# Optimization experiments

Measured on AMD Instinct MI355X. Metric: run time of the kernel, lower is better.

## Reference

```python
import jax, jax.numpy as jnp
import numpy as np

N_NODES = 50000
N_EDGES = 800000
F_IN = 128
HEADS = 4
C_OUT = 32
NEG_SLOPE = 0.2
BN_EPS = 1e-5


def _add_self_loops(edge_index, edge_attr, n):
    # PyG fill_value='mean': self-loop attr = mean of incoming edge attrs per node (0 if none)
    src, dst = edge_index[0], edge_index[1]
    deg = jax.ops.segment_sum(jnp.ones_like(edge_attr[:, 0]), dst, num_segments=n)
    loop_attr = jax.ops.segment_sum(edge_attr, dst, num_segments=n) / jnp.maximum(deg, 1.0)[:, None]
    loop = jnp.arange(n)
    src2 = jnp.concatenate([src, loop])
    dst2 = jnp.concatenate([dst, loop])
    attr2 = jnp.concatenate([edge_attr, loop_attr], axis=0)
    return src2, dst2, attr2


def _segment_softmax(logits, seg, n):
    m = jax.ops.segment_max(logits, seg, num_segments=n)
    m = jnp.where(jnp.isfinite(m), m, 0.0)
    ex = jnp.exp(logits - m[seg])
    s = jax.ops.segment_sum(ex, seg, num_segments=n)
    return ex / s[seg]


def _gatv2(x, src, dst, eattr, Wl, bl, Wr, br, We, att, bias, n):
    # x: [n, F]; returns [n, HEADS*C_OUT]
    xl = (x @ Wl + bl).reshape(n, HEADS, C_OUT)
    xr = (x @ Wr + br).reshape(n, HEADS, C_OUT)
    ea = (eattr @ We).reshape(-1, HEADS, C_OUT)
    xlj = xl[src]                                   # [E, H, C] gather
    msg = jax.nn.leaky_relu(xlj + xr[dst] + ea, NEG_SLOPE)
    logits = jnp.einsum('ehc,hc->eh', msg, att)     # [E, H]
    alpha = _segment_softmax(logits, dst, n)
    out = jax.ops.segment_sum(xlj * alpha[..., None], dst, num_segments=n)
    return out.reshape(n, HEADS * C_OUT) + bias


def _batchnorm(x, gamma, beta):
    mu = x.mean(axis=0)
    var = x.var(axis=0)
    return gamma * (x - mu) * jax.lax.rsqrt(var + BN_EPS) + beta


def setup_inputs() -> dict:
    key = jax.random.key(0)
    ks = jax.random.split(key, 20)
    HC = HEADS * C_OUT
    s = 0.05
    inp = {
        'emb': jax.random.normal(ks[0], (N_NODES, F_IN), dtype=jnp.float32),
        'edge_index': jax.random.randint(ks[1], (2, N_EDGES), 0, N_NODES, dtype=jnp.int64),
        'edge_weight': jax.random.uniform(ks[2], (N_EDGES, 1), dtype=jnp.float32),
        'Wl1': jax.random.normal(ks[3], (F_IN, HC)) * s,
        'bl1': jnp.zeros((HC,), jnp.float32),
        'Wr1': jax.random.normal(ks[4], (F_IN, HC)) * s,
        'br1': jnp.zeros((HC,), jnp.float32),
        'We1': jax.random.normal(ks[5], (1, HC)) * s,
        'att1': jax.random.normal(ks[6], (HEADS, C_OUT)) * s,
        'bias1': jnp.zeros((HC,), jnp.float32),
        'gamma1': jnp.ones((HC,), jnp.float32),
        'beta1': jnp.zeros((HC,), jnp.float32),
        'Wl2': jax.random.normal(ks[7], (HC, HC)) * s,
        'bl2': jnp.zeros((HC,), jnp.float32),
        'Wr2': jax.random.normal(ks[8], (HC, HC)) * s,
        'br2': jnp.zeros((HC,), jnp.float32),
        'We2': jax.random.normal(ks[9], (1, HC)) * s,
        'att2': jax.random.normal(ks[10], (HEADS, C_OUT)) * s,
        'bias2': jnp.zeros((HC,), jnp.float32),
    }
    return inp


def reference(emb, edge_index, edge_weight, Wl1, bl1, Wr1, br1, We1, att1, bias1,
              gamma1, beta1, Wl2, bl2, Wr2, br2, We2, att2, bias2):
    n = emb.shape[0]
    src, dst, eattr = _add_self_loops(edge_index, edge_weight, n)
    h1 = _gatv2(emb, src, dst, eattr, Wl1, bl1, Wr1, br1, We1, att1, bias1, n)
    h1 = jax.nn.elu(_batchnorm(h1, gamma1, beta1))
    h2 = _gatv2(h1, src, dst, eattr, Wl2, bl2, Wr2, br2, We2, att2, bias2, n)
    # fusion: mean over [input_emb, h1, h2] along stacked axis
    return (emb + h1 + h2) / 3.0
```

## Files before the change

kernel.cpp:

```cpp
#include <hip/hip_runtime.h>
#include <hip/hip_bf16.h>
#include <math.h>

#define N_NODES 50000
#define N_EDGES 800000
#define HC 128
#define SLOT 64
#define CSTRIDE 16

#define BM 128
#define NBX ((N_NODES + BM - 1) / BM)
#define NB_EDGE ((N_EDGES / 4 + 255) / 256)

typedef short bh8 __attribute__((ext_vector_type(8)));
typedef float f4 __attribute__((ext_vector_type(4)));
typedef float f2 __attribute__((ext_vector_type(2)));

__device__ __forceinline__ unsigned int pk2(float a, float b) {
  return (unsigned int)__bfloat16_as_ushort(__float2bfloat16(a)) |
         ((unsigned int)__bfloat16_as_ushort(__float2bfloat16(b)) << 16);
}
__device__ __forceinline__ float blo(unsigned int u) { return __uint_as_float(u << 16); }
__device__ __forceinline__ float bhi(unsigned int u) { return __uint_as_float(u & 0xffff0000u); }

__global__ __launch_bounds__(256) void k_wprep(
    const float* __restrict__ Wl1, const float* __restrict__ Wr1,
    const float* __restrict__ Wl2, const float* __restrict__ Wr2,
    unsigned short* __restrict__ WtAll, int* __restrict__ cursor,
    float* __restrict__ chsum, float* __restrict__ chsq) {
  int gid = blockIdx.x * 256 + threadIdx.x;
  int m = gid >> 14;
  int idx = gid & 16383;
  const float* src = (m == 0) ? Wl1 : (m == 1) ? Wr1 : (m == 2) ? Wl2 : Wr2;
  int k = idx >> 7, n = idx & 127;
  WtAll[((size_t)m * HC + n) * HC + k] =
      __bfloat16_as_ushort(__float2bfloat16(src[k * HC + n]));
  for (int i = gid; i < N_NODES * CSTRIDE; i += 65536) cursor[i] = 0;
  if (gid < HC) { chsum[gid] = 0.f; chsq[gid] = 0.f; }
}

__global__ __launch_bounds__(256) void k_g1prep(
    const float* __restrict__ X, const unsigned short* __restrict__ Wt,
    const float* __restrict__ b0, const float* __restrict__ b1,
    unsigned short* __restrict__ Y0b, float* __restrict__ Y1,
    const int* __restrict__ ei, const float* __restrict__ ew,
    int* __restrict__ cursor, unsigned int* __restrict__ slots) {
  int bid = blockIdx.x;
  int tid = threadIdx.x;
  if (bid >= NBX) {
    int e = ((bid - NBX) * 256 + tid) * 4;
    if (e >= N_EDGES) return;
    int4 s4 = *(const int4*)(ei + e);
    int4 d4 = *(const int4*)(ei + N_EDGES + e);
    float4 w4 = *(const float4*)(ew + e);
    int ss[4] = {s4.x, s4.y, s4.z, s4.w};
    int dd[4] = {d4.x, d4.y, d4.z, d4.w};
    float ww[4] = {w4.x, w4.y, w4.z, w4.w};
    int pos[4];
#pragma unroll
    for (int i = 0; i < 4; ++i) pos[i] = atomicAdd(cursor + dd[i] * CSTRIDE, 1);
#pragma unroll
    for (int i = 0; i < 4; ++i) {
      unsigned int wq = min((unsigned int)(ww[i] * 65536.f + 0.5f), 65535u);
      if (pos[i] < SLOT) {
        slots[(size_t)dd[i] * SLOT + pos[i]] = ((unsigned int)ss[i] << 16) | wq;
      }
    }
    return;
  }
  __shared__ __align__(16) unsigned short Xls[128 * 128];
  int row0 = bid * BM;
  {
    int r = tid >> 1;
    int ks = (tid & 1) * 64;
    int gr = row0 + r;
    const float* xp = X + (size_t)gr * HC + ks;
    int sw = r & 15;
#pragma unroll
    for (int i = 0; i < 4; ++i) {
      float f[16];
      if (gr < N_NODES) {
        *(float4*)&f[0] = *(const float4*)(xp + i * 16);
        *(float4*)&f[4] = *(const float4*)(xp + i * 16 + 4);
        *(float4*)&f[8] = *(const float4*)(xp + i * 16 + 8);
        *(float4*)&f[12] = *(const float4*)(xp + i * 16 + 12);
      } else {
#pragma unroll
        for (int j = 0; j < 16; ++j) f[j] = 0.f;
      }
      int kg = (ks >> 3) + i * 2;
      *(uint4*)&Xls[r * 128 + ((kg ^ sw) * 8)] =
          make_uint4(pk2(f[0], f[1]), pk2(f[2], f[3]), pk2(f[4], f[5]), pk2(f[6], f[7]));
      *(uint4*)&Xls[r * 128 + (((kg + 1) ^ sw) * 8)] =
          make_uint4(pk2(f[8], f[9]), pk2(f[10], f[11]), pk2(f[12], f[13]), pk2(f[14], f[15]));
    }
  }
  __syncthreads();
  int lane = tid & 63;
  int wv = tid >> 6;
  int lrow = lane & 15;
  int lq = lane >> 4;
  int rbase = wv * 32;
  bh8 afr[4][2];
#pragma unroll
  for (int kk = 0; kk < 4; ++kk) {
    int kg = kk * 4 + lq;
    afr[kk][0] = *(const bh8*)&Xls[(rbase + lrow) * 128 + ((kg ^ lrow) * 8)];
    afr[kk][1] = *(const bh8*)&Xls[(rbase + 16 + lrow) * 128 + ((kg ^ lrow) * 8)];
  }
#pragma unroll
  for (int half = 0; half < 2; ++half) {
    const unsigned short* wbase = Wt + half * (HC * HC);
    f4 acc[2][8];
#pragma unroll
    for (int mt = 0; mt < 2; ++mt)
#pragma unroll
      for (int nt = 0; nt < 8; ++nt) acc[mt][nt] = (f4){0.f, 0.f, 0.f, 0.f};
#pragma unroll
    for (int kk = 0; kk < 4; ++kk) {
      int kg = kk * 4 + lq;
#pragma unroll
      for (int nt = 0; nt < 8; ++nt) {
        bh8 b = *(const bh8*)(wbase + (nt * 16 + lrow) * HC + kg * 8);
        acc[0][nt] = __builtin_amdgcn_mfma_f32_16x16x32_bf16(afr[kk][0], b, acc[0][nt], 0, 0, 0);
        acc[1][nt] = __builtin_amdgcn_mfma_f32_16x16x32_bf16(afr[kk][1], b, acc[1][nt], 0, 0, 0);
      }
    }
    const float* bb = half ? b1 : b0;
    float bv[8];
#pragma unroll
    for (int nt = 0; nt < 8; ++nt) bv[nt] = bb[nt * 16 + lrow];
#pragma unroll
    for (int mt = 0; mt < 2; ++mt) {
#pragma unroll
      for (int rr = 0; rr < 4; ++rr) {
        int gr = row0 + rbase + mt * 16 + lq * 4 + rr;
        if (gr < N_NODES) {
          if (half == 0) {
#pragma unroll
            for (int nt = 0; nt < 8; ++nt)
              Y0b[(size_t)gr * HC + nt * 16 + lrow] =
                  __bfloat16_as_ushort(__float2bfloat16(acc[mt][nt][rr] + bv[nt]));
          } else {
#pragma unroll
            for (int nt = 0; nt < 8; ++nt)
              Y1[(size_t)gr * HC + nt * 16 + lrow] = acc[mt][nt][rr] + bv[nt];
          }
        }
      }
    }
  }
}

__global__ __launch_bounds__(256) void k_gemm2(
    const unsigned short* __restrict__ Xb, const unsigned short* __restrict__ Wt,
    const float* __restrict__ b0, const float* __restrict__ b1,
    unsigned char* __restrict__ Y0f8, float* __restrict__ Y1,
    const float* __restrict__ chsum, const float* __restrict__ chsq,
    const float* __restrict__ gamma, const float* __restrict__ beta) {
  __shared__ __align__(16) unsigned short Xls[128 * 128];
  __shared__ __align__(16) unsigned short Wls[128 * 128];
  __shared__ float ssc[HC], ssh[HC];
  int tid = threadIdx.x;
  if (tid < HC) {
    float mu = chsum[tid] * (1.f / N_NODES);
    float var = chsq[tid] * (1.f / N_NODES) - mu * mu;
    float sc = gamma[tid] * rsqrtf(var + 1e-5f);
    ssc[tid] = sc;
    ssh[tid] = beta[tid] - mu * sc;
  }
  __syncthreads();
  int row0 = blockIdx.x * BM;
  {
    int r = tid >> 1;
    int ks = (tid & 1) * 64;
    int gr = row0 + r;
    const unsigned short* xp = Xb + (size_t)gr * HC + ks;
    int sw = r & 15;
#pragma unroll
    for (int i = 0; i < 4; ++i) {
      float f[16];
      if (gr < N_NODES) {
        uint4 ua = *(const uint4*)(xp + i * 16);
        uint4 ub = *(const uint4*)(xp + i * 16 + 8);
        f[0] = blo(ua.x); f[1] = bhi(ua.x); f[2] = blo(ua.y); f[3] = bhi(ua.y);
        f[4] = blo(ua.z); f[5] = bhi(ua.z); f[6] = blo(ua.w); f[7] = bhi(ua.w);
        f[8] = blo(ub.x); f[9] = bhi(ub.x); f[10] = blo(ub.y); f[11] = bhi(ub.y);
        f[12] = blo(ub.z); f[13] = bhi(ub.z); f[14] = blo(ub.w); f[15] = bhi(ub.w);
      } else {
#pragma unroll
        for (int j = 0; j < 16; ++j) f[j] = 0.f;
      }
#pragma unroll
      for (int j = 0; j < 16; ++j) {
        float y = fmaf(f[j], ssc[ks + i * 16 + j], ssh[ks + i * 16 + j]);
        f[j] = (y > 0.f) ? y : (__expf(y) - 1.f);
      }
      int kg = (ks >> 3) + i * 2;
      *(uint4*)&Xls[r * 128 + ((kg ^ sw) * 8)] =
          make_uint4(pk2(f[0], f[1]), pk2(f[2], f[3]), pk2(f[4], f[5]), pk2(f[6], f[7]));
      *(uint4*)&Xls[r * 128 + (((kg + 1) ^ sw) * 8)] =
          make_uint4(pk2(f[8], f[9]), pk2(f[10], f[11]), pk2(f[12], f[13]), pk2(f[14], f[15]));
    }
  }
  int lane = tid & 63;
  int wv = tid >> 6;
  int lrow = lane & 15;
  int lq = lane >> 4;
  int rbase = wv * 32;
#pragma unroll
  for (int half = 0; half < 2; ++half) {
    if (half) __syncthreads();
    {
      int n = tid >> 1;
      int ks = (tid & 1) * 64;
      const unsigned short* wp = Wt + half * (HC * HC) + n * HC + ks;
      int swn = n & 15;
#pragma unroll
      for (int g = 0; g < 8; ++g) {
        uint4 v = *(const uint4*)(wp + g * 8);
        int kg = (ks >> 3) + g;
        *(uint4*)&Wls[n * 128 + ((kg ^ swn) * 8)] = v;
      }
    }
    __syncthreads();
    f4 acc[2][8];
#pragma unroll
    for (int mt = 0; mt < 2; ++mt)
#pragma unroll
      for (int nt = 0; nt < 8; ++nt) acc[mt][nt] = (f4){0.f, 0.f, 0.f, 0.f};
#pragma unroll
    for (int kk = 0; kk < 4; ++kk) {
      int kg = kk * 4 + lq;
      bh8 a0 = *(const bh8*)&Xls[(rbase + lrow) * 128 + ((kg ^ lrow) * 8)];
      bh8 a1 = *(const bh8*)&Xls[(rbase + 16 + lrow) * 128 + ((kg ^ lrow) * 8)];
#pragma unroll
      for (int nt = 0; nt < 8; ++nt) {
        bh8 b = *(const bh8*)&Wls[(nt * 16 + lrow) * 128 + ((kg ^ lrow) * 8)];
        acc[0][nt] = __builtin_amdgcn_mfma_f32_16x16x32_bf16(a0, b, acc[0][nt], 0, 0, 0);
        acc[1][nt] = __builtin_amdgcn_mfma_f32_16x16x32_bf16(a1, b, acc[1][nt], 0, 0, 0);
      }
    }
    const float* bb = half ? b1 : b0;
    float bv[8];
#pragma unroll
    for (int nt = 0; nt < 8; ++nt) bv[nt] = bb[nt * 16 + lrow];
#pragma unroll
    for (int mt = 0; mt < 2; ++mt) {
#pragma unroll
      for (int rr = 0; rr < 4; ++rr) {
        int gr = row0 + rbase + mt * 16 + lq * 4 + rr;
        if (gr < N_NODES) {
          if (half == 0) {
#pragma unroll
            for (int nt = 0; nt < 8; ++nt) {
              float v = acc[mt][nt][rr] + bv[nt];
              int p = __builtin_amdgcn_cvt_pk_fp8_f32(v, v, 0, false);
              Y0f8[(size_t)gr * HC + nt * 16 + lrow] = (unsigned char)(p & 0xff);
            }
          } else {
#pragma unroll
            for (int nt = 0; nt < 8; ++nt)
              Y1[(size_t)gr * HC + nt * 16 + lrow] = acc[mt][nt][rr] + bv[nt];
          }
        }
      }
    }
  }
}

template <int FINAL, int F8>
__global__ __launch_bounds__(256) void k_gat(
    const void* __restrict__ xlv, const float* __restrict__ xr,
    const int* __restrict__ cursor, const unsigned int* __restrict__ slots,
    const float* __restrict__ We, const float* __restrict__ att,
    const float* __restrict__ bias, void* __restrict__ out,
    const float* __restrict__ emb, const unsigned short* __restrict__ h1p,
    const float* __restrict__ chsum, const float* __restrict__ chsq,
    const float* __restrict__ gamma, const float* __restrict__ beta) {
  int g = threadIdx.x >> 5;
  int lane = threadIdx.x & 31;
  int n = blockIdx.x * 8 + g;
  int fi = n * 32 + lane;
  const uint2* xl2 = (const uint2*)xlv;
  const unsigned int* xf = (const unsigned int*)xlv;
  float4 xr4 = ((const float4*)xr)[fi];
  float4 we4 = ((const float4*)We)[lane];
  float4 at4 = ((const float4*)att)[lane];
  int deg = min(cursor[n * CSTRIDE], SLOT);
  int base = n * SLOT;
  int deg32 = min(deg, 32);

  unsigned int ev = (lane < deg32) ? slots[base + lane] : 0u;
  float evw = (float)(ev & 0xffffu) * (1.f / 65536.f);
  float wsum = evw;
#pragma unroll
  for (int m = 16; m >= 1; m >>= 1) wsum += __shfl_xor(wsum, m);

  float l = 0.f;
  float4 o = make_float4(0.f, 0.f, 0.f, 0.f);

  auto decode = [&](uint2 gc) -> float4 {
    float4 xlj;
    if (F8) {
      f2 ab = __builtin_amdgcn_cvt_pk_f32_fp8((int)gc.x, false);
      f2 cd = __builtin_amdgcn_cvt_pk_f32_fp8((int)gc.x, true);
      xlj.x = ab[0]; xlj.y = ab[1]; xlj.z = cd[0]; xlj.w = cd[1];
    } else {
      xlj.x = blo(gc.x); xlj.y = bhi(gc.x);
      xlj.z = blo(gc.y); xlj.w = bhi(gc.y);
    }
    return xlj;
  };
  auto edge_body = [&](float w, uint2 gc, bool valid) {
    float4 xlj = decode(gc);
    float4 v;
    v.x = fmaf(w, we4.x, xlj.x + xr4.x);
    v.y = fmaf(w, we4.y, xlj.y + xr4.y);
    v.z = fmaf(w, we4.z, xlj.z + xr4.z);
    v.w = fmaf(w, we4.w, xlj.w + xr4.w);
    v.x = fmaxf(v.x, 0.2f * v.x);
    v.y = fmaxf(v.y, 0.2f * v.y);
    v.z = fmaxf(v.z, 0.2f * v.z);
    v.w = fmaxf(v.w, 0.2f * v.w);
    float p = v.x * at4.x + v.y * at4.y + v.z * at4.z + v.w * at4.w;
    p += __shfl_xor(p, 1);
    p += __shfl_xor(p, 2);
    p += __shfl_xor(p, 4);
    float e = valid ? __expf(p) : 0.f;
    l += e;
    o.x = fmaf(e, xlj.x, o.x);
    o.y = fmaf(e, xlj.y, o.y);
    o.z = fmaf(e, xlj.z, o.z);
    o.w = fmaf(e, xlj.w, o.w);
  };
  auto fetch = [&](int j, uint2& qq, float& ww) {
    int jc = min(j, deg32 - 1);
    unsigned int evj = __shfl(ev, jc, 32);
    ww = (float)(evj & 0xffffu) * (1.f / 65536.f);
    int s = (int)(evj >> 16);
    if (F8) qq.x = xf[s * 32 + lane];
    else qq = xl2[s * 32 + lane];
  };

  if (deg32 > 0) {
    uint2 q0, q1, q2, q3;
    float w0, w1, w2, w3;
    fetch(0, q0, w0);
    fetch(1, q1, w1);
    fetch(2, q2, w2);
    fetch(3, q3, w3);
    for (int b = 0; b < deg32; b += 4) {
      uint2 c0 = q0, c1 = q1, c2 = q2, c3 = q3;
      float x0 = w0, x1 = w1, x2 = w2, x3 = w3;
      fetch(b + 4, q0, w0);
      fetch(b + 5, q1, w1);
      fetch(b + 6, q2, w2);
      fetch(b + 7, q3, w3);
      edge_body(x0, c0, true);
      edge_body(x1, c1, b + 1 < deg32);
      edge_body(x2, c2, b + 2 < deg32);
      edge_body(x3, c3, b + 3 < deg32);
    }
  }
  if (deg > 32) {
    for (int j = base + 32; j < base + deg; ++j) {
      unsigned int evj = slots[j];
      float w = (float)(evj & 0xffffu) * (1.f / 65536.f);
      wsum += w;
      int s = (int)(evj >> 16);
      uint2 gc;
      if (F8) gc.x = xf[s * 32 + lane];
      else gc = xl2[s * 32 + lane];
      edge_body(w, gc, true);
    }
  }
  {
    float wself = (deg > 0) ? wsum / (float)deg : 0.f;
    uint2 gs;
    if (F8) gs.x = xf[n * 32 + lane];
    else gs = xl2[n * 32 + lane];
    edge_body(wself, gs, true);
  }

  float inv = 1.f / l;
  float4 b4 = ((const float4*)bias)[lane];
  float4 r;
  r.x = fmaf(o.x, inv, b4.x);
  r.y = fmaf(o.y, inv, b4.y);
  r.z = fmaf(o.z, inv, b4.z);
  r.w = fmaf(o.w, inv, b4.w);
  if (FINAL) {
    float4 e4 = ((const float4*)emb)[fi];
    uint2 hh = ((const uint2*)h1p)[fi];
    float4 h4;
    h4.x = blo(hh.x); h4.y = bhi(hh.x); h4.z = blo(hh.y); h4.w = bhi(hh.y);
    float4 cs = ((const float4*)chsum)[lane];
    float4 cq = ((const float4*)chsq)[lane];
    float4 gm = ((const float4*)gamma)[lane];
    float4 bt = ((const float4*)beta)[lane];
    const float invN = 1.f / N_NODES;
    float4 sc4, sh4;
    {
      float mu = cs.x * invN, var = cq.x * invN - mu * mu;
      sc4.x = gm.x * rsqrtf(var + 1e-5f); sh4.x = bt.x - mu * sc4.x;
      mu = cs.y * invN; var = cq.y * invN - mu * mu;
      sc4.y = gm.y * rsqrtf(var + 1e-5f); sh4.y = bt.y - mu * sc4.y;
      mu = cs.z * invN; var = cq.z * invN - mu * mu;
      sc4.z = gm.z * rsqrtf(var + 1e-5f); sh4.z = bt.z - mu * sc4.z;
      mu = cs.w * invN; var = cq.w * invN - mu * mu;
      sc4.w = gm.w * rsqrtf(var + 1e-5f); sh4.w = bt.w - mu * sc4.w;
    }
    float4 h;
    h.x = fmaf(h4.x, sc4.x, sh4.x);
    h.y = fmaf(h4.y, sc4.y, sh4.y);
    h.z = fmaf(h4.z, sc4.z, sh4.z);
    h.w = fmaf(h4.w, sc4.w, sh4.w);
    h.x = (h.x > 0.f) ? h.x : (__expf(h.x) - 1.f);
    h.y = (h.y > 0.f) ? h.y : (__expf(h.y) - 1.f);
    h.z = (h.z > 0.f) ? h.z : (__expf(h.z) - 1.f);
    h.w = (h.w > 0.f) ? h.w : (__expf(h.w) - 1.f);
    const float k3 = 1.f / 3.f;
    r.x = (e4.x + h.x + r.x) * k3;
    r.y = (e4.y + h.y + r.y) * k3;
    r.z = (e4.z + h.z + r.z) * k3;
    r.w = (e4.w + h.w + r.w) * k3;
    ((float4*)out)[fi] = r;
  } else {
    ((uint2*)out)[fi] = make_uint2(pk2(r.x, r.y), pk2(r.z, r.w));
  }
}

#define BN_ROWS 200
__global__ __launch_bounds__(256) void k_bnstats(const unsigned short* __restrict__ h1b,
                                                 float* __restrict__ chsum,
                                                 float* __restrict__ chsq) {
  int c2 = threadIdx.x & 63;
  int g = threadIdx.x >> 6;
  int r0 = blockIdx.x * BN_ROWS;
  float s0 = 0.f, s1 = 0.f, q0 = 0.f, q1 = 0.f;
  const unsigned int* h32 = (const unsigned int*)h1b;
  for (int r = r0 + g; r < r0 + BN_ROWS; r += 4) {
    unsigned int u = h32[(size_t)r * 64 + c2];
    float a = blo(u), b = bhi(u);
    s0 += a; q0 += a * a;
    s1 += b; q1 += b * b;
  }
  __shared__ float sh[256][4];
  sh[threadIdx.x][0] = s0; sh[threadIdx.x][1] = q0;
  sh[threadIdx.x][2] = s1; sh[threadIdx.x][3] = q1;
  __syncthreads();
  if (g == 0) {
    float ts0 = 0.f, tq0 = 0.f, ts1 = 0.f, tq1 = 0.f;
#pragma unroll
    for (int gg = 0; gg < 4; ++gg) {
      ts0 += sh[gg * 64 + c2][0]; tq0 += sh[gg * 64 + c2][1];
      ts1 += sh[gg * 64 + c2][2]; tq1 += sh[gg * 64 + c2][3];
    }
    atomicAdd(chsum + 2 * c2, ts0);
    atomicAdd(chsq + 2 * c2, tq0);
    atomicAdd(chsum + 2 * c2 + 1, ts1);
    atomicAdd(chsq + 2 * c2 + 1, tq1);
  }
}

extern "C" void kernel_launch(void* const* d_in, const int* in_sizes, int n_in,
                              void* d_out, int out_size, void* d_ws, size_t ws_size,
                              hipStream_t stream) {
  const float* emb = (const float*)d_in[0];
  const int* ei = (const int*)d_in[1];
  const float* ew = (const float*)d_in[2];
  const float* Wl1 = (const float*)d_in[3];
  const float* bl1 = (const float*)d_in[4];
  const float* Wr1 = (const float*)d_in[5];
  const float* br1 = (const float*)d_in[6];
  const float* We1 = (const float*)d_in[7];
  const float* att1 = (const float*)d_in[8];
  const float* bias1 = (const float*)d_in[9];
  const float* gamma1 = (const float*)d_in[10];
  const float* beta1 = (const float*)d_in[11];
  const float* Wl2 = (const float*)d_in[12];
  const float* bl2 = (const float*)d_in[13];
  const float* Wr2 = (const float*)d_in[14];
  const float* br2 = (const float*)d_in[15];
  const float* We2 = (const float*)d_in[16];
  const float* att2 = (const float*)d_in[17];
  const float* bias2 = (const float*)d_in[18];
  float* out = (float*)d_out;

  char* wsb = (char*)d_ws;
  size_t off = 0;
  auto alloc = [&](size_t bytes) -> void* {
    void* p = (void*)(wsb + off);
    off += (bytes + 255) & ~(size_t)255;
    return p;
  };
  int* cursor = (int*)alloc((size_t)N_NODES * CSTRIDE * 4);
  float* chsum = (float*)alloc(HC * 4);
  float* chsq = (float*)alloc(HC * 4);
  unsigned short* WtAll = (unsigned short*)alloc((size_t)4 * HC * HC * 2);
  unsigned int* slots = (unsigned int*)alloc((size_t)N_NODES * SLOT * 4);
  unsigned short* xlb = (unsigned short*)alloc((size_t)N_NODES * HC * 2);
  unsigned char* xlf8 = (unsigned char*)alloc((size_t)N_NODES * HC);
  float* xr = (float*)alloc((size_t)N_NODES * HC * 4);
  unsigned short* h1b = (unsigned short*)alloc((size_t)N_NODES * HC * 2);

  k_wprep<<<256, 256, 0, stream>>>(Wl1, Wr1, Wl2, Wr2, WtAll, cursor, chsum, chsq);
  k_g1prep<<<NBX + NB_EDGE, 256, 0, stream>>>(emb, WtAll, bl1, br1, xlb, xr,
                                              ei, ew, cursor, slots);
  k_gat<0, 0><<<N_NODES / 8, 256, 0, stream>>>(xlb, xr, cursor, slots, We1, att1,
                                               bias1, (void*)h1b, nullptr, nullptr,
                                               nullptr, nullptr, nullptr, nullptr);
  k_bnstats<<<N_NODES / BN_ROWS, 256, 0, stream>>>(h1b, chsum, chsq);
  k_gemm2<<<NBX, 256, 0, stream>>>(h1b, WtAll + 2 * HC * HC, bl2, br2, xlf8, xr,
                                   chsum, chsq, gamma1, beta1);
  k_gat<1, 1><<<N_NODES / 8, 256, 0, stream>>>(xlf8, xr, cursor, slots, We2, att2,
                                               bias2, (void*)out, emb, h1b,
                                               chsum, chsq, gamma1, beta1);
}
```

Before: 289.9 us.

## Fuse edge bucketing into GEMM blocks and stage weights in LDS

Removes the separate edge-processing blocks of the first prep kernel. Each GEMM thread now handles 8 edges, issuing its cursor atomics before the X tile load so their latency overlaps with the tile staging, and writing slots afterward. Weight tiles are staged into swizzled shared memory per half instead of being loaded from global memory per MFMA, and A fragments are reloaded from LDS per k-step. LDS usage doubles to 64KB per block, which may limit occupancy, and every GEMM thread now carries the serialized atomic work.

```diff
diff --git a/kernel.cpp b/kernel.cpp
--- a/kernel.cpp
+++ b/kernel.cpp
@@ -10,7 +10,6 @@
 
 #define BM 128
 #define NBX ((N_NODES + BM - 1) / BM)
-#define NB_EDGE ((N_EDGES / 4 + 255) / 256)
 
 typedef short bh8 __attribute__((ext_vector_type(8)));
 typedef float f4 __attribute__((ext_vector_type(4)));
@@ -45,30 +44,28 @@
     unsigned short* __restrict__ Y0b, float* __restrict__ Y1,
     const int* __restrict__ ei, const float* __restrict__ ew,
     int* __restrict__ cursor, unsigned int* __restrict__ slots) {
+  __shared__ __align__(16) unsigned short Xls[128 * 128];
+  __shared__ __align__(16) unsigned short Wls[128 * 128];
   int bid = blockIdx.x;
   int tid = threadIdx.x;
-  if (bid >= NBX) {
-    int e = ((bid - NBX) * 256 + tid) * 4;
-    if (e >= N_EDGES) return;
-    int4 s4 = *(const int4*)(ei + e);
-    int4 d4 = *(const int4*)(ei + N_EDGES + e);
-    float4 w4 = *(const float4*)(ew + e);
-    int ss[4] = {s4.x, s4.y, s4.z, s4.w};
-    int dd[4] = {d4.x, d4.y, d4.z, d4.w};
-    float ww[4] = {w4.x, w4.y, w4.z, w4.w};
-    int pos[4];
-#pragma unroll
-    for (int i = 0; i < 4; ++i) pos[i] = atomicAdd(cursor + dd[i] * CSTRIDE, 1);
-#pragma unroll
-    for (int i = 0; i < 4; ++i) {
-      unsigned int wq = min((unsigned int)(ww[i] * 65536.f + 0.5f), 65535u);
-      if (pos[i] < SLOT) {
-        slots[(size_t)dd[i] * SLOT + pos[i]] = ((unsigned int)ss[i] << 16) | wq;
-      }
-    }
-    return;
-  }
-  __shared__ __align__(16) unsigned short Xls[128 * 128];
+
+  int et = bid * 256 + tid;
+  bool has_e = (et < N_EDGES / 8);
+  int e0 = et * 8;
+  int ss[8], dd[8];
+  float ww[8];
+  int pos[8];
+  if (has_e) {
+    *(int4*)&ss[0] = *(const int4*)(ei + e0);
+    *(int4*)&ss[4] = *(const int4*)(ei + e0 + 4);
+    *(int4*)&dd[0] = *(const int4*)(ei + N_EDGES + e0);
+    *(int4*)&dd[4] = *(const int4*)(ei + N_EDGES + e0 + 4);
+    *(float4*)&ww[0] = *(const float4*)(ew + e0);
+    *(float4*)&ww[4] = *(const float4*)(ew + e0 + 4);
+#pragma unroll
+    for (int i = 0; i < 8; ++i) pos[i] = atomicAdd(cursor + dd[i] * CSTRIDE, 1);
+  }
+
   int row0 = bid * BM;
   {
     int r = tid >> 1;
@@ -95,22 +92,38 @@
           make_uint4(pk2(f[8], f[9]), pk2(f[10], f[11]), pk2(f[12], f[13]), pk2(f[14], f[15]));
     }
   }
-  __syncthreads();
+
+  if (has_e) {
+#pragma unroll
+    for (int i = 0; i < 8; ++i) {
+      unsigned int wq = min((unsigned int)(ww[i] * 65536.f + 0.5f), 65535u);
+      if (pos[i] < SLOT) {
+        slots[(size_t)dd[i] * SLOT + pos[i]] = ((unsigned int)ss[i] << 16) | wq;
+      }
+    }
+  }
+
   int lane = tid & 63;
   int wv = tid >> 6;
   int lrow = lane & 15;
   int lq = lane >> 4;
   int rbase = wv * 32;
-  bh8 afr[4][2];
-#pragma unroll
-  for (int kk = 0; kk < 4; ++kk) {
-    int kg = kk * 4 + lq;
-    afr[kk][0] = *(const bh8*)&Xls[(rbase + lrow) * 128 + ((kg ^ lrow) * 8)];
-    afr[kk][1] = *(const bh8*)&Xls[(rbase + 16 + lrow) * 128 + ((kg ^ lrow) * 8)];
-  }
 #pragma unroll
   for (int half = 0; half < 2; ++half) {
-    const unsigned short* wbase = Wt + half * (HC * HC);
+    if (half) __syncthreads();
+    {
+      int n = tid >> 1;
+      int ks2 = (tid & 1) * 64;
+      const unsigned short* wp = Wt + half * (HC * HC) + n * HC + ks2;
+      int swn = n & 15;
+#pragma unroll
+      for (int g = 0; g < 8; ++g) {
+        uint4 v = *(const uint4*)(wp + g * 8);
+        int kg = (ks2 >> 3) + g;
+        *(uint4*)&Wls[n * 128 + ((kg ^ swn) * 8)] = v;
+      }
+    }
+    __syncthreads();
     f4 acc[2][8];
 #pragma unroll
     for (int mt = 0; mt < 2; ++mt)
@@ -119,11 +132,13 @@
 #pragma unroll
     for (int kk = 0; kk < 4; ++kk) {
       int kg = kk * 4 + lq;
+      bh8 a0 = *(const bh8*)&Xls[(rbase + lrow) * 128 + ((kg ^ lrow) * 8)];
+      bh8 a1 = *(const bh8*)&Xls[(rbase + 16 + lrow) * 128 + ((kg ^ lrow) * 8)];
 #pragma unroll
       for (int nt = 0; nt < 8; ++nt) {
-        bh8 b = *(const bh8*)(wbase + (nt * 16 + lrow) * HC + kg * 8);
-        acc[0][nt] = __builtin_amdgcn_mfma_f32_16x16x32_bf16(afr[kk][0], b, acc[0][nt], 0, 0, 0);
-        acc[1][nt] = __builtin_amdgcn_mfma_f32_16x16x32_bf16(afr[kk][1], b, acc[1][nt], 0, 0, 0);
+        bh8 b = *(const bh8*)&Wls[(nt * 16 + lrow) * 128 + ((kg ^ lrow) * 8)];
+        acc[0][nt] = __builtin_amdgcn_mfma_f32_16x16x32_bf16(a0, b, acc[0][nt], 0, 0, 0);
+        acc[1][nt] = __builtin_amdgcn_mfma_f32_16x16x32_bf16(a1, b, acc[1][nt], 0, 0, 0);
       }
     }
     const float* bb = half ? b1 : b0;
@@ -506,8 +521,8 @@
   unsigned short* h1b = (unsigned short*)alloc((size_t)N_NODES * HC * 2);
 
   k_wprep<<<256, 256, 0, stream>>>(Wl1, Wr1, Wl2, Wr2, WtAll, cursor, chsum, chsq);
-  k_g1prep<<<NBX + NB_EDGE, 256, 0, stream>>>(emb, WtAll, bl1, br1, xlb, xr,
-                                              ei, ew, cursor, slots);
+  k_g1prep<<<NBX, 256, 0, stream>>>(emb, WtAll, bl1, br1, xlb, xr,
+                                    ei, ew, cursor, slots);
   k_gat<0, 0><<<N_NODES / 8, 256, 0, stream>>>(xlb, xr, cursor, slots, We1, att1,
                                                bias1, (void*)h1b, nullptr, nullptr,
                                                nullptr, nullptr, nullptr, nullptr);
```

Measured after the change: 295.2 us. About the same (+1.8%).
